# Performance work log

Hardware: AMD Instinct MI355X
Metric: run time of the kernel (lower is better)

Reference implementation:

```python
import jax, jax.numpy as jnp
import numpy as np

B, T, F, C = 1024, 64, 1024, 3  # batch, num_trees, num_features, num_of_cls
NSLOT, N2 = 5, 16


def setup_inputs() -> dict:
    key = jax.random.key(0)
    ks = jax.random.split(key, 9)
    return {
        "d": jax.random.normal(ks[0], (B, 2048), jnp.float32),
        "idx": jax.random.randint(ks[1], (T, F), 0, 2048, jnp.int32),
        "cc": jax.random.randint(ks[2], (T, C), 0, NSLOT, jnp.int32),
        "w_clc": jax.random.normal(ks[3], (T, F, 2), jnp.float32) * 0.02,
        "b_clc": jax.random.normal(ks[4], (T, 2), jnp.float32) * 0.02,
        "w1": jax.random.normal(ks[5], (T, F, C), jnp.float32) * 0.02,
        "b1": jax.random.normal(ks[6], (T, C), jnp.float32) * 0.02,
        "w2": jax.random.normal(ks[7], (T, F + C, N2), jnp.float32) * 0.02,
        "b2": jax.random.normal(ks[8], (T, N2), jnp.float32) * 0.02,
    }


def reference(d, idx, cc, w_clc, b_clc, w1, b1, w2, b2):
    # Per-tree random feature gather: [B, T, F]
    g = d[:, idx]
    # Gate: clc[i](d[:, idx[i]]).log_softmax(-1)
    w = jax.nn.log_softmax(jnp.einsum('btf,tfc->btc', g, w_clc) + b_clc, axis=-1)
    # AgentCLS (eval mode: dropout = identity)
    logits1 = jnp.einsum('btf,tfc->btc', g, w1) + b1          # [B,T,C]
    y1 = jax.nn.log_softmax(logits1, axis=-1)
    x2 = jnp.concatenate([g, jax.nn.relu(logits1)], axis=-1)  # [B,T,F+C]
    y2 = jax.nn.log_softmax(jnp.einsum('btf,tfc->btc', x2, w2) + b2, axis=-1)
    # Gate-weighted scatter combine (get_output math)
    gate = jnp.exp(w[..., 1:2])                               # [B,T,1]
    onehot = jax.nn.one_hot(cc, NSLOT, dtype=d.dtype)         # [T,C,5]
    out5 = jnp.einsum('btc,tcx->bx', jnp.exp(y1) * gate, onehot)
    count5 = jnp.einsum('bt,tx->bx', gate[..., 0], onehot.sum(1))
    out5 = jnp.where(count5 > 0, out5 / jnp.where(count5 > 0, count5, 1.0), 0.0)
    gsum = gate.sum(1)                                        # [B,1]
    out16 = (jnp.exp(y2) * gate).sum(1) / gsum
    return jnp.concatenate([out5, out16], axis=-1)            # [B,21]
```

## Files before the change

### kernel.cpp

```cpp
#include <hip/hip_runtime.h>

#define NT 64
#define NF 1024
#define NB 1024
#define ND 2048
#define NTP 32
#define NN2 (NT * NTP)
#define NP 27
#define NW2ROW 1027
#define BK 64
#define BM 64
#define BN 64

typedef __attribute__((ext_vector_type(8))) short short8;
typedef __attribute__((ext_vector_type(4))) float f32x4;

static __device__ __forceinline__ unsigned short f2bf(float x) {
    unsigned u = __float_as_uint(x);
    unsigned r = (u + 0x7FFFu + ((u >> 16) & 1u)) >> 16;
    return (unsigned short)r;
}

__global__ __launch_bounds__(1024) void prep_kernel(
    const int* __restrict__ idx, const float* __restrict__ w_clc,
    const float* __restrict__ w1, const float* __restrict__ w2,
    const float* __restrict__ d, unsigned short* __restrict__ Wf,
    unsigned short* __restrict__ db)
{
    __shared__ __align__(16) float tile[21 * 256];
    int bid = blockIdx.x;
    int tid = threadIdx.x;

    if (bid < 512) {
        int t = bid >> 3, je = bid & 7;

        float4* tz = (float4*)tile;
        for (int i = tid; i < 1344; i += 1024) tz[i] = make_float4(0, 0, 0, 0);
        __syncthreads();

        {
            int f = tid;
            int j = idx[t * NF + f];
            if ((j >> 8) == je) {
                int jl = j & 255;
                float2 a = *(const float2*)&w_clc[(size_t)(t * NF + f) * 2];
                atomicAdd(&tile[0 * 256 + jl], a.x);
                atomicAdd(&tile[1 * 256 + jl], a.y);
                const float* p1 = &w1[(size_t)(t * NF + f) * 3];
                atomicAdd(&tile[2 * 256 + jl], p1[0]);
                atomicAdd(&tile[3 * 256 + jl], p1[1]);
                atomicAdd(&tile[4 * 256 + jl], p1[2]);
                const float* w2row = &w2[((size_t)t * NW2ROW + f) * 16];
                float4 q0 = *(const float4*)&w2row[0];
                float4 q1 = *(const float4*)&w2row[4];
                float4 q2 = *(const float4*)&w2row[8];
                float4 q3 = *(const float4*)&w2row[12];
                atomicAdd(&tile[ 5 * 256 + jl], q0.x);
                atomicAdd(&tile[ 6 * 256 + jl], q0.y);
                atomicAdd(&tile[ 7 * 256 + jl], q0.z);
                atomicAdd(&tile[ 8 * 256 + jl], q0.w);
                atomicAdd(&tile[ 9 * 256 + jl], q1.x);
                atomicAdd(&tile[10 * 256 + jl], q1.y);
                atomicAdd(&tile[11 * 256 + jl], q1.z);
                atomicAdd(&tile[12 * 256 + jl], q1.w);
                atomicAdd(&tile[13 * 256 + jl], q2.x);
                atomicAdd(&tile[14 * 256 + jl], q2.y);
                atomicAdd(&tile[15 * 256 + jl], q2.z);
                atomicAdd(&tile[16 * 256 + jl], q2.w);
                atomicAdd(&tile[17 * 256 + jl], q3.x);
                atomicAdd(&tile[18 * 256 + jl], q3.y);
                atomicAdd(&tile[19 * 256 + jl], q3.z);
                atomicAdd(&tile[20 * 256 + jl], q3.w);
            }
        }
        __syncthreads();

        for (int i = tid; i < 672; i += 1024) {
            int c = i >> 5, off = (i & 31) * 8;
            const float* tr = &tile[c * 256 + off];
            union { unsigned short u[8]; uint4 v; } pk;
#pragma unroll
            for (int e = 0; e < 8; ++e) pk.u[e] = f2bf(tr[e]);
            *(uint4*)&Wf[(size_t)(t * NTP + c) * ND + je * 256 + off] = pk.v;
        }
        uint4 z = make_uint4(0, 0, 0, 0);
        for (int i = tid; i < 352; i += 1024) {
            int c = 21 + (i >> 5), off = (i & 31) * 8;
            *(uint4*)&Wf[(size_t)(t * NTP + c) * ND + je * 256 + off] = z;
        }
    } else {
        int cb = bid - 512;
        int i16 = (cb * 1024 + tid) * 16;
#pragma unroll
        for (int h = 0; h < 2; ++h) {
            int i8 = i16 + h * 8;
            float4 a = *(const float4*)&d[i8];
            float4 b = *(const float4*)&d[i8 + 4];
            union { unsigned short u[8]; uint4 v; } pk;
            pk.u[0] = f2bf(a.x); pk.u[1] = f2bf(a.y); pk.u[2] = f2bf(a.z); pk.u[3] = f2bf(a.w);
            pk.u[4] = f2bf(b.x); pk.u[5] = f2bf(b.y); pk.u[6] = f2bf(b.z); pk.u[7] = f2bf(b.w);
            *(uint4*)&db[i8] = pk.v;
        }
    }
}

__global__ __launch_bounds__(256, 2) void fused_kernel(
    const unsigned short* __restrict__ A,
    const unsigned short* __restrict__ Bm,
    const float* __restrict__ b_clc, const float* __restrict__ b1,
    const float* __restrict__ b2, const float* __restrict__ w2,
    const int* __restrict__ cc, float* __restrict__ ptl2)
{
    __shared__ __align__(16) char smem[32768];
    unsigned short (*As)[BM][BK] = (unsigned short(*)[BM][BK])smem;
    unsigned short (*Bs)[BN][BK] = (unsigned short(*)[BN][BK])(smem + 16384);
    float* Cl  = (float*)smem;
    float* red = (float*)(smem + 16896);

    int tid = threadIdx.x;
    int lane = tid & 63;
    int wv = tid >> 6;
    int wr = wv & 1;
    int wq = wv >> 1;
    int nb = blockIdx.x;
    int mb = blockIdx.y;
    int m0 = mb * BM;
    int n0 = nb * BN;
    int r0 = lane & 15;
    int kq = lane >> 4;
    int sx = r0 & 7;
    int sl0 = ((0 * 4 + kq) ^ sx) * 8;
    int sl1 = ((1 * 4 + kq) ^ sx) * 8;

    f32x4 acc[2][2];
#pragma unroll
    for (int mi = 0; mi < 2; ++mi)
#pragma unroll
        for (int ni = 0; ni < 2; ++ni) acc[mi][ni] = (f32x4)0.f;

#define STAGE(buf, kt)                                                          \
    {                                                                           \
        size_t koff = (size_t)(kt) * BK;                                        \
        _Pragma("unroll")                                                       \
        for (int p = 0; p < 2; ++p) {                                           \
            int chunk = p * 256 + tid;                                          \
            int row = chunk >> 3, c = chunk & 7;                                \
            int csw = (c ^ (row & 7)) * 8;                                      \
            const unsigned short* ga = A + (size_t)(m0 + row) * ND + koff + csw;\
            __builtin_amdgcn_global_load_lds(                                   \
                (const __attribute__((address_space(1))) void*)ga,              \
                (__attribute__((address_space(3))) void*)&As[buf][row][c * 8],  \
                16, 0, 0);                                                      \
        }                                                                       \
        _Pragma("unroll")                                                       \
        for (int p = 0; p < 2; ++p) {                                           \
            int chunk = p * 256 + tid;                                          \
            int row = chunk >> 3, c = chunk & 7;                                \
            int csw = (c ^ (row & 7)) * 8;                                      \
            const unsigned short* gb = Bm + (size_t)(n0 + row) * ND + koff + csw;\
            __builtin_amdgcn_global_load_lds(                                   \
                (const __attribute__((address_space(1))) void*)gb,              \
                (__attribute__((address_space(3))) void*)&Bs[buf][row][c * 8],  \
                16, 0, 0);                                                      \
        }                                                                       \
    }

    STAGE(0, 0);

    int cur = 0;
    for (int kt = 0; kt < 32; ++kt) {
        if (kt < 31) {
            STAGE(cur ^ 1, kt + 1);
            asm volatile("s_waitcnt vmcnt(4)" ::: "memory");
        } else {
            asm volatile("s_waitcnt vmcnt(0)" ::: "memory");
        }
        __builtin_amdgcn_s_barrier();
        __builtin_amdgcn_sched_barrier(0);

        short8 af[2][2], bf[2][2];
#pragma unroll
        for (int mi = 0; mi < 2; ++mi) {
            af[mi][0] = *(const short8*)&As[cur][wr*32 + mi*16 + r0][sl0];
            af[mi][1] = *(const short8*)&As[cur][wr*32 + mi*16 + r0][sl1];
        }
#pragma unroll
        for (int ni = 0; ni < 2; ++ni) {
            bf[ni][0] = *(const short8*)&Bs[cur][wq*32 + ni*16 + r0][sl0];
            bf[ni][1] = *(const short8*)&Bs[cur][wq*32 + ni*16 + r0][sl1];
        }
#pragma unroll
        for (int ks = 0; ks < 2; ++ks)
#pragma unroll
            for (int mi = 0; mi < 2; ++mi)
#pragma unroll
                for (int ni = 0; ni < 2; ++ni)
                    acc[mi][ni] = __builtin_amdgcn_mfma_f32_16x16x32_bf16(
                        af[mi][ks], bf[ni][ks], acc[mi][ni], 0, 0, 0);

        __builtin_amdgcn_sched_barrier(0);
        __builtin_amdgcn_s_barrier();
        __builtin_amdgcn_sched_barrier(0);
        cur ^= 1;
    }
#undef STAGE

#pragma unroll
    for (int mi = 0; mi < 2; ++mi)
#pragma unroll
        for (int ni = 0; ni < 2; ++ni) {
            int n = wq * 32 + ni * 16 + r0;
            int bl = wr * 32 + mi * 16 + kq * 4;
#pragma unroll
            for (int q = 0; q < 4; ++q)
                Cl[(bl + q) * 65 + n] = acc[mi][ni][q];
        }
    __syncthreads();

    int tl = tid >> 6;
    int bl = lane;
    float s[NP];
#pragma unroll
    for (int k = 0; k < NP; ++k) s[k] = 0.f;

    if (tl < 2) {
        int t = nb * 2 + tl;

        float a21[21];
#pragma unroll
        for (int k = 0; k < 21; ++k) a21[k] = Cl[bl * 65 + tl * 32 + k];

        float L0 = a21[0] + b_clc[t * 2 + 0];
        float L1 = a21[1] + b_clc[t * 2 + 1];
        float mm = fmaxf(L0, L1);
        float e0 = __expf(L0 - mm), e1 = __expf(L1 - mm);
        float gate = e1 / (e0 + e1);

        float l1v[3];
        float m1 = -3.0e38f;
#pragma unroll
        for (int c = 0; c < 3; ++c) {
            l1v[c] = a21[2 + c] + b1[t * 3 + c];
            m1 = fmaxf(m1, l1v[c]);
        }
        float p1[3]; float S1 = 0.f;
#pragma unroll
        for (int c = 0; c < 3; ++c) { p1[c] = __expf(l1v[c] - m1); S1 += p1[c]; }
        float invS1g = gate / S1;

        float r0f = fmaxf(l1v[0], 0.f);
        float r1f = fmaxf(l1v[1], 0.f);
        float r2f = fmaxf(l1v[2], 0.f);

        const float* w2t = w2 + ((size_t)t * NW2ROW + NF) * 16;
        float l2[16]; float m2 = -3.0e38f;
#pragma unroll
        for (int nn = 0; nn < 16; ++nn) {
            float v = a21[5 + nn] + b2[t * 16 + nn];
            v = fmaf(r0f, w2t[nn], v);
            v = fmaf(r1f, w2t[16 + nn], v);
            v = fmaf(r2f, w2t[32 + nn], v);
            l2[nn] = v;
            m2 = fmaxf(m2, v);
        }
        float S2 = 0.f; float p2[16];
#pragma unroll
        for (int nn = 0; nn < 16; ++nn) { p2[nn] = __expf(l2[nn] - m2); S2 += p2[nn]; }
        float invS2g = gate * __frcp_rn(S2);

#pragma unroll
        for (int c = 0; c < 3; ++c) {
            int sl = cc[t * 3 + c];
            float pc = p1[c] * invS1g;
#pragma unroll
            for (int x = 0; x < 5; ++x) {
                if (sl == x) { s[x] += pc; s[5 + x] += gate; }
            }
        }
#pragma unroll
        for (int nn = 0; nn < 16; ++nn) s[10 + nn] += p2[nn] * invS2g;
        s[26] += gate;
    }

    if (tl == 1) {
#pragma unroll
        for (int k = 0; k < NP; ++k) red[k * 64 + bl] = s[k];
    }
    __syncthreads();
    if (tl != 0) return;

#pragma unroll
    for (int k = 0; k < NP; ++k) s[k] += red[k * 64 + bl];

    float* pt = ptl2 + (size_t)nb * NP * NB + m0 + bl;
#pragma unroll
    for (int k = 0; k < NP; ++k)
        pt[(size_t)k * NB] = s[k];
}

__global__ __launch_bounds__(1024) void finalize_kernel(
    const float* __restrict__ ptl2, float* __restrict__ out)
{
    __shared__ float red[8][NP][64];
    int lane = threadIdx.x & 63;
    int w = threadIdx.x >> 6;
    int b = blockIdx.x * 64 + lane;

    float s[NP];
#pragma unroll
    for (int k = 0; k < NP; ++k) s[k] = 0.f;
#pragma unroll
    for (int i = 0; i < 2; ++i) {
        const float* pt = ptl2 + (size_t)(w * 2 + i) * NP * NB + b;
#pragma unroll
        for (int k = 0; k < NP; ++k) s[k] += pt[(size_t)k * NB];
    }

    if (w >= 8) {
#pragma unroll
        for (int k = 0; k < NP; ++k) red[w - 8][k][lane] = s[k];
    }
    __syncthreads();
    if (w < 8) {
#pragma unroll
        for (int k = 0; k < NP; ++k) s[k] += red[w][k][lane];
    }
    __syncthreads();
    if (w >= 4 && w < 8) {
#pragma unroll
        for (int k = 0; k < NP; ++k) red[w - 4][k][lane] = s[k];
    }
    __syncthreads();
    if (w < 4) {
#pragma unroll
        for (int k = 0; k < NP; ++k) s[k] += red[w][k][lane];
    }
    __syncthreads();
    if (w >= 2 && w < 4) {
#pragma unroll
        for (int k = 0; k < NP; ++k) red[w - 2][k][lane] = s[k];
    }
    __syncthreads();
    if (w < 2) {
#pragma unroll
        for (int k = 0; k < NP; ++k) s[k] += red[w][k][lane];
    }
    __syncthreads();
    if (w == 1) {
#pragma unroll
        for (int k = 0; k < NP; ++k) red[0][k][lane] = s[k];
    }
    __syncthreads();
    if (w != 0) return;
#pragma unroll
    for (int k = 0; k < NP; ++k) s[k] += red[0][k][lane];

    float* ob = out + (size_t)b * 21;
#pragma unroll
    for (int x = 0; x < 5; ++x) {
        float c = s[5 + x];
        ob[x] = (c > 0.f) ? (s[x] / c) : 0.f;
    }
    float invg = 1.f / s[26];
#pragma unroll
    for (int n = 0; n < 16; ++n) ob[5 + n] = s[10 + n] * invg;
}

extern "C" void kernel_launch(void* const* d_in, const int* in_sizes, int n_in,
                              void* d_out, int out_size, void* d_ws, size_t ws_size,
                              hipStream_t stream)
{
    const float* d     = (const float*)d_in[0];
    const int*   idx   = (const int*)  d_in[1];
    const int*   cc    = (const int*)  d_in[2];
    const float* w_clc = (const float*)d_in[3];
    const float* b_clc = (const float*)d_in[4];
    const float* w1    = (const float*)d_in[5];
    const float* b1    = (const float*)d_in[6];
    const float* w2    = (const float*)d_in[7];
    const float* b2    = (const float*)d_in[8];
    float* out = (float*)d_out;

    unsigned short* Wf = (unsigned short*)d_ws;
    unsigned short* db = Wf + (size_t)NN2 * ND;
    float* ptl2 = (float*)(db + (size_t)NB * ND);

    prep_kernel<<<640, 1024, 0, stream>>>(idx, w_clc, w1, w2, d, Wf, db);
    fused_kernel<<<dim3(32, 16), 256, 0, stream>>>(db, Wf, b_clc, b1, b2, w2, cc, ptl2);
    finalize_kernel<<<16, 1024, 0, stream>>>(ptl2, out);
}
```

Baseline: 38.89 us.

## Split K across waves with 128-wide K tiles and LDS reduction

The GEMM main loop now uses a K tile of 128, doubling the shared memory staging buffers to 64KB, and halves the number of K iterations. Each wave computes the full 64x64 output tile over its own quarter of K instead of a 32x32 quadrant over all of K. The partial results are then combined with a two-level reduction through shared memory before the epilogue. This cuts barriers and loop overhead per K step and lets each wave reuse more fragments per load, at the cost of 64 accumulator registers per lane, extra reduction syncs, and doubled LDS that may lower occupancy.

```diff
diff --git a/kernel.cpp b/kernel.cpp
--- a/kernel.cpp
+++ b/kernel.cpp
@@ -8,7 +8,7 @@
 #define NN2 (NT * NTP)
 #define NP 27
 #define NW2ROW 1027
-#define BK 64
+#define BKK 128
 #define BM 64
 #define BN 64
 
@@ -111,41 +111,39 @@
     const float* __restrict__ b2, const float* __restrict__ w2,
     const int* __restrict__ cc, float* __restrict__ ptl2)
 {
-    __shared__ __align__(16) char smem[32768];
-    unsigned short (*As)[BM][BK] = (unsigned short(*)[BM][BK])smem;
-    unsigned short (*Bs)[BN][BK] = (unsigned short(*)[BN][BK])(smem + 16384);
-    float* Cl  = (float*)smem;
-    float* red = (float*)(smem + 16896);
+    __shared__ __align__(16) char smem[65536];
+    unsigned short (*As)[BM][BKK] = (unsigned short(*)[BM][BKK])smem;
+    unsigned short (*Bs)[BN][BKK] = (unsigned short(*)[BN][BKK])(smem + 32768);
+    float* s0  = (float*)smem;
+    float* s1  = s0 + 64 * 66;
+    float* Cl  = s1 + 64 * 66;
+    float* red = Cl + 64 * 66;
 
     int tid = threadIdx.x;
     int lane = tid & 63;
     int wv = tid >> 6;
-    int wr = wv & 1;
-    int wq = wv >> 1;
     int nb = blockIdx.x;
     int mb = blockIdx.y;
     int m0 = mb * BM;
     int n0 = nb * BN;
     int r0 = lane & 15;
     int kq = lane >> 4;
-    int sx = r0 & 7;
-    int sl0 = ((0 * 4 + kq) ^ sx) * 8;
-    int sl1 = ((1 * 4 + kq) ^ sx) * 8;
-
-    f32x4 acc[2][2];
-#pragma unroll
-    for (int mi = 0; mi < 2; ++mi)
-#pragma unroll
-        for (int ni = 0; ni < 2; ++ni) acc[mi][ni] = (f32x4)0.f;
+    int slotbase = wv * 4 + kq;
+
+    f32x4 acc[4][4];
+#pragma unroll
+    for (int mi = 0; mi < 4; ++mi)
+#pragma unroll
+        for (int ni = 0; ni < 4; ++ni) acc[mi][ni] = (f32x4)0.f;
 
 #define STAGE(buf, kt)                                                          \
     {                                                                           \
-        size_t koff = (size_t)(kt) * BK;                                        \
+        size_t koff = (size_t)(kt) * BKK;                                       \
         _Pragma("unroll")                                                       \
-        for (int p = 0; p < 2; ++p) {                                           \
+        for (int p = 0; p < 4; ++p) {                                           \
             int chunk = p * 256 + tid;                                          \
-            int row = chunk >> 3, c = chunk & 7;                                \
-            int csw = (c ^ (row & 7)) * 8;                                      \
+            int row = chunk >> 4, c = chunk & 15;                               \
+            int csw = (c ^ (row & 15)) * 8;                                     \
             const unsigned short* ga = A + (size_t)(m0 + row) * ND + koff + csw;\
             __builtin_amdgcn_global_load_lds(                                   \
                 (const __attribute__((address_space(1))) void*)ga,              \
@@ -153,10 +151,10 @@
                 16, 0, 0);                                                      \
         }                                                                       \
         _Pragma("unroll")                                                       \
-        for (int p = 0; p < 2; ++p) {                                           \
+        for (int p = 0; p < 4; ++p) {                                           \
             int chunk = p * 256 + tid;                                          \
-            int row = chunk >> 3, c = chunk & 7;                                \
-            int csw = (c ^ (row & 7)) * 8;                                      \
+            int row = chunk >> 4, c = chunk & 15;                               \
+            int csw = (c ^ (row & 15)) * 8;                                     \
             const unsigned short* gb = Bm + (size_t)(n0 + row) * ND + koff + csw;\
             __builtin_amdgcn_global_load_lds(                                   \
                 (const __attribute__((address_space(1))) void*)gb,              \
@@ -168,35 +166,29 @@
     STAGE(0, 0);
 
     int cur = 0;
-    for (int kt = 0; kt < 32; ++kt) {
-        if (kt < 31) {
+    for (int kt = 0; kt < 16; ++kt) {
+        if (kt < 15) {
             STAGE(cur ^ 1, kt + 1);
-            asm volatile("s_waitcnt vmcnt(4)" ::: "memory");
+            asm volatile("s_waitcnt vmcnt(8)" ::: "memory");
         } else {
             asm volatile("s_waitcnt vmcnt(0)" ::: "memory");
         }
         __builtin_amdgcn_s_barrier();
         __builtin_amdgcn_sched_barrier(0);
 
-        short8 af[2][2], bf[2][2];
-#pragma unroll
-        for (int mi = 0; mi < 2; ++mi) {
-            af[mi][0] = *(const short8*)&As[cur][wr*32 + mi*16 + r0][sl0];
-            af[mi][1] = *(const short8*)&As[cur][wr*32 + mi*16 + r0][sl1];
-        }
-#pragma unroll
-        for (int ni = 0; ni < 2; ++ni) {
-            bf[ni][0] = *(const short8*)&Bs[cur][wq*32 + ni*16 + r0][sl0];
-            bf[ni][1] = *(const short8*)&Bs[cur][wq*32 + ni*16 + r0][sl1];
-        }
-#pragma unroll
-        for (int ks = 0; ks < 2; ++ks)
-#pragma unroll
-            for (int mi = 0; mi < 2; ++mi)
-#pragma unroll
-                for (int ni = 0; ni < 2; ++ni)
-                    acc[mi][ni] = __builtin_amdgcn_mfma_f32_16x16x32_bf16(
-                        af[mi][ks], bf[ni][ks], acc[mi][ni], 0, 0, 0);
+        short8 af[4], bf[4];
+#pragma unroll
+        for (int mi = 0; mi < 4; ++mi)
+            af[mi] = *(const short8*)&As[cur][mi * 16 + r0][(slotbase ^ r0) * 8];
+#pragma unroll
+        for (int ni = 0; ni < 4; ++ni)
+            bf[ni] = *(const short8*)&Bs[cur][ni * 16 + r0][(slotbase ^ r0) * 8];
+#pragma unroll
+        for (int mi = 0; mi < 4; ++mi)
+#pragma unroll
+            for (int ni = 0; ni < 4; ++ni)
+                acc[mi][ni] = __builtin_amdgcn_mfma_f32_16x16x32_bf16(
+                    af[mi], bf[ni], acc[mi][ni], 0, 0, 0);
 
         __builtin_amdgcn_sched_barrier(0);
         __builtin_amdgcn_s_barrier();
@@ -205,16 +197,49 @@
     }
 #undef STAGE
 
-#pragma unroll
-    for (int mi = 0; mi < 2; ++mi)
-#pragma unroll
-        for (int ni = 0; ni < 2; ++ni) {
-            int n = wq * 32 + ni * 16 + r0;
-            int bl = wr * 32 + mi * 16 + kq * 4;
-#pragma unroll
-            for (int q = 0; q < 4; ++q)
-                Cl[(bl + q) * 65 + n] = acc[mi][ni][q];
-        }
+    if (wv >= 2) {
+        float* dst = (wv == 2) ? s0 : s1;
+#pragma unroll
+        for (int mi = 0; mi < 4; ++mi)
+#pragma unroll
+            for (int ni = 0; ni < 4; ++ni)
+#pragma unroll
+                for (int q = 0; q < 4; ++q)
+                    dst[(mi * 16 + kq * 4 + q) * 66 + ni * 16 + r0] = acc[mi][ni][q];
+    }
+    __syncthreads();
+    if (wv < 2) {
+        const float* src = (wv == 0) ? s0 : s1;
+#pragma unroll
+        for (int mi = 0; mi < 4; ++mi)
+#pragma unroll
+            for (int ni = 0; ni < 4; ++ni)
+#pragma unroll
+                for (int q = 0; q < 4; ++q)
+                    acc[mi][ni][q] += src[(mi * 16 + kq * 4 + q) * 66 + ni * 16 + r0];
+    }
+    __syncthreads();
+    if (wv == 1) {
+#pragma unroll
+        for (int mi = 0; mi < 4; ++mi)
+#pragma unroll
+            for (int ni = 0; ni < 4; ++ni)
+#pragma unroll
+                for (int q = 0; q < 4; ++q)
+                    s0[(mi * 16 + kq * 4 + q) * 66 + ni * 16 + r0] = acc[mi][ni][q];
+    }
+    __syncthreads();
+    if (wv == 0) {
+#pragma unroll
+        for (int mi = 0; mi < 4; ++mi)
+#pragma unroll
+            for (int ni = 0; ni < 4; ++ni)
+#pragma unroll
+                for (int q = 0; q < 4; ++q) {
+                    float v = acc[mi][ni][q] + s0[(mi * 16 + kq * 4 + q) * 66 + ni * 16 + r0];
+                    Cl[(mi * 16 + kq * 4 + q) * 66 + ni * 16 + r0] = v;
+                }
+    }
     __syncthreads();
 
     int tl = tid >> 6;
@@ -228,7 +253,7 @@
 
         float a21[21];
 #pragma unroll
-        for (int k = 0; k < 21; ++k) a21[k] = Cl[bl * 65 + tl * 32 + k];
+        for (int k = 0; k < 21; ++k) a21[k] = Cl[bl * 66 + tl * 32 + k];
 
         float L0 = a21[0] + b_clc[t * 2 + 0];
         float L1 = a21[1] + b_clc[t * 2 + 1];
```

Measured after the change: 41.90 us. 1.08x slower.

## Triple-buffer GEMM LDS pipeline and fold input bf16 conversion into prep blocks

Applied to the files above, without the earlier changes.

The fused GEMM moves from a double-buffered to a triple-buffered LDS pipeline. Two stages are prefetched up front and each iteration issues the load two steps ahead, so the per-iteration trailing barrier goes away and load latency gets more cover. This raises LDS use to 48KB per block, which may limit occupancy. The prep kernel also drops its separate blocks for converting d to bf16: each of the 512 weight-scatter blocks now converts a slice of d, loaded early so it overlaps the atomic scatter, and the grid shrinks to 512 blocks.

```diff
diff --git a/kernel.cpp b/kernel.cpp
--- a/kernel.cpp
+++ b/kernel.cpp
@@ -31,76 +31,71 @@
     int bid = blockIdx.x;
     int tid = threadIdx.x;
 
-    if (bid < 512) {
-        int t = bid >> 3, je = bid & 7;
-
-        float4* tz = (float4*)tile;
-        for (int i = tid; i < 1344; i += 1024) tz[i] = make_float4(0, 0, 0, 0);
-        __syncthreads();
-
-        {
-            int f = tid;
-            int j = idx[t * NF + f];
-            if ((j >> 8) == je) {
-                int jl = j & 255;
-                float2 a = *(const float2*)&w_clc[(size_t)(t * NF + f) * 2];
-                atomicAdd(&tile[0 * 256 + jl], a.x);
-                atomicAdd(&tile[1 * 256 + jl], a.y);
-                const float* p1 = &w1[(size_t)(t * NF + f) * 3];
-                atomicAdd(&tile[2 * 256 + jl], p1[0]);
-                atomicAdd(&tile[3 * 256 + jl], p1[1]);
-                atomicAdd(&tile[4 * 256 + jl], p1[2]);
-                const float* w2row = &w2[((size_t)t * NW2ROW + f) * 16];
-                float4 q0 = *(const float4*)&w2row[0];
-                float4 q1 = *(const float4*)&w2row[4];
-                float4 q2 = *(const float4*)&w2row[8];
-                float4 q3 = *(const float4*)&w2row[12];
-                atomicAdd(&tile[ 5 * 256 + jl], q0.x);
-                atomicAdd(&tile[ 6 * 256 + jl], q0.y);
-                atomicAdd(&tile[ 7 * 256 + jl], q0.z);
-                atomicAdd(&tile[ 8 * 256 + jl], q0.w);
-                atomicAdd(&tile[ 9 * 256 + jl], q1.x);
-                atomicAdd(&tile[10 * 256 + jl], q1.y);
-                atomicAdd(&tile[11 * 256 + jl], q1.z);
-                atomicAdd(&tile[12 * 256 + jl], q1.w);
-                atomicAdd(&tile[13 * 256 + jl], q2.x);
-                atomicAdd(&tile[14 * 256 + jl], q2.y);
-                atomicAdd(&tile[15 * 256 + jl], q2.z);
-                atomicAdd(&tile[16 * 256 + jl], q2.w);
-                atomicAdd(&tile[17 * 256 + jl], q3.x);
-                atomicAdd(&tile[18 * 256 + jl], q3.y);
-                atomicAdd(&tile[19 * 256 + jl], q3.z);
-                atomicAdd(&tile[20 * 256 + jl], q3.w);
-            }
-        }
-        __syncthreads();
-
-        for (int i = tid; i < 672; i += 1024) {
-            int c = i >> 5, off = (i & 31) * 8;
-            const float* tr = &tile[c * 256 + off];
-            union { unsigned short u[8]; uint4 v; } pk;
-#pragma unroll
-            for (int e = 0; e < 8; ++e) pk.u[e] = f2bf(tr[e]);
-            *(uint4*)&Wf[(size_t)(t * NTP + c) * ND + je * 256 + off] = pk.v;
-        }
-        uint4 z = make_uint4(0, 0, 0, 0);
-        for (int i = tid; i < 352; i += 1024) {
-            int c = 21 + (i >> 5), off = (i & 31) * 8;
-            *(uint4*)&Wf[(size_t)(t * NTP + c) * ND + je * 256 + off] = z;
-        }
-    } else {
-        int cb = bid - 512;
-        int i16 = (cb * 1024 + tid) * 16;
-#pragma unroll
-        for (int h = 0; h < 2; ++h) {
-            int i8 = i16 + h * 8;
-            float4 a = *(const float4*)&d[i8];
-            float4 b = *(const float4*)&d[i8 + 4];
-            union { unsigned short u[8]; uint4 v; } pk;
-            pk.u[0] = f2bf(a.x); pk.u[1] = f2bf(a.y); pk.u[2] = f2bf(a.z); pk.u[3] = f2bf(a.w);
-            pk.u[4] = f2bf(b.x); pk.u[5] = f2bf(b.y); pk.u[6] = f2bf(b.z); pk.u[7] = f2bf(b.w);
-            *(uint4*)&db[i8] = pk.v;
-        }
+    int i4 = (bid * 1024 + tid) * 4;
+    float4 cv = *(const float4*)&d[i4];
+
+    int t = bid >> 3, je = bid & 7;
+
+    float4* tz = (float4*)tile;
+    for (int i = tid; i < 1344; i += 1024) tz[i] = make_float4(0, 0, 0, 0);
+    __syncthreads();
+
+    {
+        int f = tid;
+        int j = idx[t * NF + f];
+        if ((j >> 8) == je) {
+            int jl = j & 255;
+            float2 a = *(const float2*)&w_clc[(size_t)(t * NF + f) * 2];
+            atomicAdd(&tile[0 * 256 + jl], a.x);
+            atomicAdd(&tile[1 * 256 + jl], a.y);
+            const float* p1 = &w1[(size_t)(t * NF + f) * 3];
+            atomicAdd(&tile[2 * 256 + jl], p1[0]);
+            atomicAdd(&tile[3 * 256 + jl], p1[1]);
+            atomicAdd(&tile[4 * 256 + jl], p1[2]);
+            const float* w2row = &w2[((size_t)t * NW2ROW + f) * 16];
+            float4 q0 = *(const float4*)&w2row[0];
+            float4 q1 = *(const float4*)&w2row[4];
+            float4 q2 = *(const float4*)&w2row[8];
+            float4 q3 = *(const float4*)&w2row[12];
+            atomicAdd(&tile[ 5 * 256 + jl], q0.x);
+            atomicAdd(&tile[ 6 * 256 + jl], q0.y);
+            atomicAdd(&tile[ 7 * 256 + jl], q0.z);
+            atomicAdd(&tile[ 8 * 256 + jl], q0.w);
+            atomicAdd(&tile[ 9 * 256 + jl], q1.x);
+            atomicAdd(&tile[10 * 256 + jl], q1.y);
+            atomicAdd(&tile[11 * 256 + jl], q1.z);
+            atomicAdd(&tile[12 * 256 + jl], q1.w);
+            atomicAdd(&tile[13 * 256 + jl], q2.x);
+            atomicAdd(&tile[14 * 256 + jl], q2.y);
+            atomicAdd(&tile[15 * 256 + jl], q2.z);
+            atomicAdd(&tile[16 * 256 + jl], q2.w);
+            atomicAdd(&tile[17 * 256 + jl], q3.x);
+            atomicAdd(&tile[18 * 256 + jl], q3.y);
+            atomicAdd(&tile[19 * 256 + jl], q3.z);
+            atomicAdd(&tile[20 * 256 + jl], q3.w);
+        }
+    }
+
+    {
+        union { unsigned short u[4]; uint2 v; } pk;
+        pk.u[0] = f2bf(cv.x); pk.u[1] = f2bf(cv.y);
+        pk.u[2] = f2bf(cv.z); pk.u[3] = f2bf(cv.w);
+        *(uint2*)&db[i4] = pk.v;
+    }
+    __syncthreads();
+
+    for (int i = tid; i < 672; i += 1024) {
+        int c = i >> 5, off = (i & 31) * 8;
+        const float* tr = &tile[c * 256 + off];
+        union { unsigned short u[8]; uint4 v; } pk;
+#pragma unroll
+        for (int e = 0; e < 8; ++e) pk.u[e] = f2bf(tr[e]);
+        *(uint4*)&Wf[(size_t)(t * NTP + c) * ND + je * 256 + off] = pk.v;
+    }
+    uint4 z = make_uint4(0, 0, 0, 0);
+    for (int i = tid; i < 352; i += 1024) {
+        int c = 21 + (i >> 5), off = (i & 31) * 8;
+        *(uint4*)&Wf[(size_t)(t * NTP + c) * ND + je * 256 + off] = z;
     }
 }
 
@@ -111,9 +106,9 @@
     const float* __restrict__ b2, const float* __restrict__ w2,
     const int* __restrict__ cc, float* __restrict__ ptl2)
 {
-    __shared__ __align__(16) char smem[32768];
+    __shared__ __align__(16) char smem[49152];
     unsigned short (*As)[BM][BK] = (unsigned short(*)[BM][BK])smem;
-    unsigned short (*Bs)[BN][BK] = (unsigned short(*)[BN][BK])(smem + 16384);
+    unsigned short (*Bs)[BN][BK] = (unsigned short(*)[BN][BK])(smem + 24576);
     float* Cl  = (float*)smem;
     float* red = (float*)(smem + 16896);
 
@@ -166,15 +161,14 @@
     }
 
     STAGE(0, 0);
-
-    int cur = 0;
+    STAGE(1, 1);
+
     for (int kt = 0; kt < 32; ++kt) {
-        if (kt < 31) {
-            STAGE(cur ^ 1, kt + 1);
+        int cur = kt % 3;
+        if (kt < 31)
             asm volatile("s_waitcnt vmcnt(4)" ::: "memory");
-        } else {
+        else
             asm volatile("s_waitcnt vmcnt(0)" ::: "memory");
-        }
         __builtin_amdgcn_s_barrier();
         __builtin_amdgcn_sched_barrier(0);
 
@@ -199,11 +193,11 @@
                         af[mi][ks], bf[ni][ks], acc[mi][ni], 0, 0, 0);
 
         __builtin_amdgcn_sched_barrier(0);
-        __builtin_amdgcn_s_barrier();
+        if (kt < 30) STAGE((kt + 2) % 3, kt + 2);
         __builtin_amdgcn_sched_barrier(0);
-        cur ^= 1;
     }
 #undef STAGE
+    __builtin_amdgcn_s_barrier();
 
 #pragma unroll
     for (int mi = 0; mi < 2; ++mi)
@@ -385,7 +379,7 @@
     unsigned short* db = Wf + (size_t)NN2 * ND;
     float* ptl2 = (float*)(db + (size_t)NB * ND);
 
-    prep_kernel<<<640, 1024, 0, stream>>>(idx, w_clc, w1, w2, d, Wf, db);
+    prep_kernel<<<512, 1024, 0, stream>>>(idx, w_clc, w1, w2, d, Wf, db);
     fused_kernel<<<dim3(32, 16), 256, 0, stream>>>(db, Wf, b_clc, b1, b2, w2, cc, ptl2);
     finalize_kernel<<<16, 1024, 0, stream>>>(ptl2, out);
 }
```

Result: slower. 40.26 us (+3.5%).

## Fuse finalize reduction into GEMM kernel via last-block atomic ticket

Applied to the files above, without the earlier changes.

Removes the separate finalize kernel launch. Each fused block writes its partial sums, fences, and increments a per-row-block counter. The last of the 32 column blocks for a row block then reduces all partials and writes the output. The counters are zeroed in prep_kernel. This saves one launch and its dependency gap, at the cost of fences, an atomic per block, and a serial tail reduction in the last block.

```diff
diff --git a/kernel.cpp b/kernel.cpp
--- a/kernel.cpp
+++ b/kernel.cpp
@@ -25,11 +25,13 @@
     const int* __restrict__ idx, const float* __restrict__ w_clc,
     const float* __restrict__ w1, const float* __restrict__ w2,
     const float* __restrict__ d, unsigned short* __restrict__ Wf,
-    unsigned short* __restrict__ db)
+    unsigned short* __restrict__ db, int* __restrict__ counters)
 {
     __shared__ __align__(16) float tile[21 * 256];
     int bid = blockIdx.x;
     int tid = threadIdx.x;
+
+    if (bid == 0 && tid < 16) counters[tid] = 0;
 
     if (bid < 512) {
         int t = bid >> 3, je = bid & 7;
@@ -109,13 +111,15 @@
     const unsigned short* __restrict__ Bm,
     const float* __restrict__ b_clc, const float* __restrict__ b1,
     const float* __restrict__ b2, const float* __restrict__ w2,
-    const int* __restrict__ cc, float* __restrict__ ptl2)
+    const int* __restrict__ cc, float* __restrict__ ptl2,
+    int* __restrict__ counters, float* __restrict__ out)
 {
     __shared__ __align__(16) char smem[32768];
     unsigned short (*As)[BM][BK] = (unsigned short(*)[BM][BK])smem;
     unsigned short (*Bs)[BN][BK] = (unsigned short(*)[BN][BK])(smem + 16384);
     float* Cl  = (float*)smem;
     float* red = (float*)(smem + 16896);
+    __shared__ int ticket;
 
     int tid = threadIdx.x;
     int lane = tid & 63;
@@ -166,6 +170,7 @@
     }
 
     STAGE(0, 0);
+    __syncthreads();
 
     int cur = 0;
     for (int kt = 0; kt < 32; ++kt) {
@@ -287,83 +292,50 @@
         for (int k = 0; k < NP; ++k) red[k * 64 + bl] = s[k];
     }
     __syncthreads();
-    if (tl != 0) return;
-
-#pragma unroll
-    for (int k = 0; k < NP; ++k) s[k] += red[k * 64 + bl];
-
-    float* pt = ptl2 + (size_t)nb * NP * NB + m0 + bl;
-#pragma unroll
-    for (int k = 0; k < NP; ++k)
-        pt[(size_t)k * NB] = s[k];
-}
-
-__global__ __launch_bounds__(1024) void finalize_kernel(
-    const float* __restrict__ ptl2, float* __restrict__ out)
-{
-    __shared__ float red[8][NP][64];
-    int lane = threadIdx.x & 63;
-    int w = threadIdx.x >> 6;
-    int b = blockIdx.x * 64 + lane;
-
-    float s[NP];
-#pragma unroll
-    for (int k = 0; k < NP; ++k) s[k] = 0.f;
-#pragma unroll
-    for (int i = 0; i < 2; ++i) {
-        const float* pt = ptl2 + (size_t)(w * 2 + i) * NP * NB + b;
-#pragma unroll
-        for (int k = 0; k < NP; ++k) s[k] += pt[(size_t)k * NB];
-    }
-
-    if (w >= 8) {
-#pragma unroll
-        for (int k = 0; k < NP; ++k) red[w - 8][k][lane] = s[k];
-    }
-    __syncthreads();
-    if (w < 8) {
-#pragma unroll
-        for (int k = 0; k < NP; ++k) s[k] += red[w][k][lane];
-    }
-    __syncthreads();
-    if (w >= 4 && w < 8) {
-#pragma unroll
-        for (int k = 0; k < NP; ++k) red[w - 4][k][lane] = s[k];
-    }
-    __syncthreads();
-    if (w < 4) {
-#pragma unroll
-        for (int k = 0; k < NP; ++k) s[k] += red[w][k][lane];
-    }
-    __syncthreads();
-    if (w >= 2 && w < 4) {
-#pragma unroll
-        for (int k = 0; k < NP; ++k) red[w - 2][k][lane] = s[k];
-    }
-    __syncthreads();
-    if (w < 2) {
-#pragma unroll
-        for (int k = 0; k < NP; ++k) s[k] += red[w][k][lane];
-    }
-    __syncthreads();
-    if (w == 1) {
-#pragma unroll
-        for (int k = 0; k < NP; ++k) red[0][k][lane] = s[k];
-    }
-    __syncthreads();
-    if (w != 0) return;
-#pragma unroll
-    for (int k = 0; k < NP; ++k) s[k] += red[0][k][lane];
-
-    float* ob = out + (size_t)b * 21;
-#pragma unroll
-    for (int x = 0; x < 5; ++x) {
-        float c = s[5 + x];
-        ob[x] = (c > 0.f) ? (s[x] / c) : 0.f;
-    }
-    float invg = 1.f / s[26];
-#pragma unroll
-    for (int n = 0; n < 16; ++n) ob[5 + n] = s[10 + n] * invg;
+    if (tl == 0) {
+#pragma unroll
+        for (int k = 0; k < NP; ++k) s[k] += red[k * 64 + bl];
+        float* pt = ptl2 + (size_t)nb * NP * NB + m0 + bl;
+#pragma unroll
+        for (int k = 0; k < NP; ++k)
+            pt[(size_t)k * NB] = s[k];
+    }
+
+    __threadfence();
+    __syncthreads();
+    if (tid == 0) ticket = atomicAdd(&counters[mb], 1);
+    __syncthreads();
+    if (ticket != 31) return;
+    __threadfence();
+
+    {
+        int b = m0 + lane;
+        for (int k = tl; k < NP; k += 4) {
+            float acc2 = 0.f;
+            const float* p = ptl2 + (size_t)k * NB + b;
+#pragma unroll 8
+            for (int nb2 = 0; nb2 < 32; ++nb2)
+                acc2 += p[(size_t)nb2 * NP * NB];
+            red[k * 64 + lane] = acc2;
+        }
+    }
+    __syncthreads();
+    if (tid < 64) {
+        int b = m0 + tid;
+        float sf[NP];
+#pragma unroll
+        for (int k = 0; k < NP; ++k) sf[k] = red[k * 64 + tid];
+
+        float* ob = out + (size_t)b * 21;
+#pragma unroll
+        for (int x = 0; x < 5; ++x) {
+            float c = sf[5 + x];
+            ob[x] = (c > 0.f) ? (sf[x] / c) : 0.f;
+        }
+        float invg = 1.f / sf[26];
+#pragma unroll
+        for (int n = 0; n < 16; ++n) ob[5 + n] = sf[10 + n] * invg;
+    }
 }
 
 extern "C" void kernel_launch(void* const* d_in, const int* in_sizes, int n_in,
@@ -384,8 +356,9 @@
     unsigned short* Wf = (unsigned short*)d_ws;
     unsigned short* db = Wf + (size_t)NN2 * ND;
     float* ptl2 = (float*)(db + (size_t)NB * ND);
-
-    prep_kernel<<<640, 1024, 0, stream>>>(idx, w_clc, w1, w2, d, Wf, db);
-    fused_kernel<<<dim3(32, 16), 256, 0, stream>>>(db, Wf, b_clc, b1, b2, w2, cc, ptl2);
-    finalize_kernel<<<16, 1024, 0, stream>>>(ptl2, out);
+    int* counters = (int*)(ptl2 + (size_t)32 * NP * NB);
+
+    prep_kernel<<<640, 1024, 0, stream>>>(idx, w_clc, w1, w2, d, Wf, db, counters);
+    fused_kernel<<<dim3(32, 16), 256, 0, stream>>>(db, Wf, b_clc, b1, b2, w2, cc,
+                                                   ptl2, counters, out);
 }
```

New measurement: 102.6 us. +163.8%, slower.
